# Kernel optimization log

Hardware: AMD Instinct MI355X
Metric: run time of the kernel (lower is better)

Reference implementation:

```python
import jax, jax.numpy as jnp
import numpy as np

T, D = 2048, 1024      # tokens, hidden_size
FF = 512               # moe_intermediate_size
E, K = 16, 4           # num_experts, top_k
L = 3                  # conv_L_cache (short causal conv width)
EPS = 1e-5
SCALE = 1.0            # routed_scaling_factor


def setup_inputs() -> dict:
    key = jax.random.key(0)
    ks = jax.random.split(key, 10)
    s = lambda k, shape, sc: jax.random.normal(k, shape, jnp.float32) * sc
    return {
        "hidden_states": s(ks[0], (T, D), 1.0),
        "residual": s(ks[1], (T, D), 1.0),
        "op_norm_w": jnp.ones((D,), jnp.float32),
        "ffn_norm_w": jnp.ones((D,), jnp.float32),
        "in_proj_w": s(ks[2], (3 * D, D), 0.02),   # produces B, C, x
        "conv_w": s(ks[3], (D, L), 0.2),            # depthwise causal kernel
        "out_proj_w": s(ks[4], (D, D), 0.02),
        "gate_w": s(ks[5], (E, D), 0.02),
        "gate_bias": s(ks[6], (E,), 0.1),           # e_score_correction_bias
        "w1": s(ks[7], (E, 2 * FF, D), 0.02),       # per-expert gate+up
        "w2": s(ks[8], (E, D, FF), 0.02),           # per-expert down
    }


def _fused_add_rmsnorm(x, w, res):
    # vLLM RMSNorm(x, residual): x += residual; residual = x; out = rmsnorm(x)*w
    x = x + res
    res = x
    v = jnp.mean(x * x, axis=-1, keepdims=True)
    return x * jax.lax.rsqrt(v + EPS) * w, res


def reference(hidden_states, residual, op_norm_w, ffn_norm_w, in_proj_w,
              conv_w, out_proj_w, gate_w, gate_bias, w1, w2):
    h, residual = _fused_add_rmsnorm(hidden_states, op_norm_w, residual)

    # ---- ShortConv mixer: Bx = B*x, causal depthwise conv, gate by C ----
    bcx = h @ in_proj_w.T                         # [T, 3D]
    B, C, x = jnp.split(bcx, 3, axis=-1)
    Bx = B * x
    xp = jnp.pad(Bx, ((L - 1, 0), (0, 0)))        # causal left-pad
    shifts = jnp.stack([xp[k:k + T] for k in range(L)], axis=0)  # [L,T,D]
    conv = jnp.einsum('ltd,dl->td', shifts, conv_w)
    y = (C * conv) @ out_proj_w.T                 # [T, D]

    h, residual = _fused_add_rmsnorm(y, ffn_norm_w, residual)

    # ---- Sparse MoE: sigmoid scoring + bias-corrected top-k, renormalize ----
    logits = h.astype(jnp.float32) @ gate_w.T     # [T, E]
    scores = jax.nn.sigmoid(logits)
    choice = scores + gate_bias                   # selection uses biased scores
    _, topi = jax.lax.top_k(choice, K)            # [T, K]
    w = jnp.take_along_axis(scores, topi, axis=-1)  # weights from raw scores
    w = w / (jnp.sum(w, axis=-1, keepdims=True) + 1e-20)  # norm_topk_prob
    cw = jnp.sum(jax.nn.one_hot(topi, E, dtype=h.dtype) * w[..., None].astype(h.dtype), axis=1)  # [T, E]

    # dense dispatch (reference): all experts on all tokens, masked combine
    gu = jnp.einsum('td,efd->etf', h, w1)         # [E, T, 2FF]
    g, u = jnp.split(gu, 2, axis=-1)
    act = jax.nn.silu(g) * u                      # SiluAndMul
    ye = jnp.einsum('etf,edf->etd', act, w2)      # [E, T, D]
    out = jnp.einsum('te,etd->td', cw, ye) * SCALE
    return out, residual
```

## Files before the change

kernel.cpp:

```cpp
#include <hip/hip_runtime.h>
#include <hip/hip_bf16.h>

#define T_  2048
#define D_  1024
#define FF_ 512
#define E_  16
#define K_  4
#define L_  3
static constexpr float EPS = 1e-5f;

typedef __hip_bfloat16 bf16;
typedef __attribute__((ext_vector_type(8))) short bf16x8;
typedef __attribute__((ext_vector_type(4))) float f32x4;

__device__ __forceinline__ float b2f(bf16 x) { return __bfloat162float(x); }

__device__ __forceinline__ unsigned int pk2(float a, float b) {
    __hip_bfloat162 h = __float22bfloat162_rn(make_float2(a, b));
    unsigned int u; __builtin_memcpy(&u, &h, 4); return u;
}

__device__ __forceinline__ void gload_lds16(const bf16* g, bf16* l) {
    __builtin_amdgcn_global_load_lds(
        (const __attribute__((address_space(1))) unsigned int*)g,
        (__attribute__((address_space(3))) unsigned int*)l, 16, 0, 0);
}

__device__ __forceinline__ void split_pack(float4 v, uint2 &hi, uint2 &lo) {
    __hip_bfloat162 h01 = __float22bfloat162_rn(make_float2(v.x, v.y));
    __hip_bfloat162 h23 = __float22bfloat162_rn(make_float2(v.z, v.w));
    float2 r01 = make_float2(v.x - __bfloat162float(h01.x), v.y - __bfloat162float(h01.y));
    float2 r23 = make_float2(v.z - __bfloat162float(h23.x), v.w - __bfloat162float(h23.y));
    __hip_bfloat162 l01 = __float22bfloat162_rn(r01);
    __hip_bfloat162 l23 = __float22bfloat162_rn(r23);
    __builtin_memcpy(&hi.x, &h01, 4); __builtin_memcpy(&hi.y, &h23, 4);
    __builtin_memcpy(&lo.x, &l01, 4); __builtin_memcpy(&lo.y, &l23, 4);
}

__global__ __launch_bounds__(256) void k_convert(const float* __restrict__ w1,
                                                 const float* __restrict__ w2,
                                                 const float* __restrict__ ipw,
                                                 const float* __restrict__ opw,
                                                 bf16* __restrict__ w1b,
                                                 bf16* __restrict__ w2b,
                                                 bf16* __restrict__ iph,
                                                 bf16* __restrict__ ipl,
                                                 bf16* __restrict__ oph,
                                                 bf16* __restrict__ opl) {
    const size_t n1 = (size_t)E_ * 2 * FF_ * D_;
    const size_t n2 = (size_t)E_ * D_ * FF_;
    const size_t n3 = (size_t)3 * D_ * D_;
    const size_t n4 = (size_t)D_ * D_;
    size_t i = ((size_t)blockIdx.x * 256 + threadIdx.x) * 4;
    if (i < n1) {
        float4 v = *(const float4*)&w1[i];
        uint2 h; h.x = pk2(v.x, v.y); h.y = pk2(v.z, v.w);
        *(uint2*)&w1b[i] = h;
    } else if (i < n1 + n2) {
        size_t j = i - n1;
        float4 v = *(const float4*)&w2[j];
        uint2 h; h.x = pk2(v.x, v.y); h.y = pk2(v.z, v.w);
        *(uint2*)&w2b[j] = h;
    } else if (i < n1 + n2 + n3) {
        size_t j = i - n1 - n2;
        float4 v = *(const float4*)&ipw[j];
        uint2 hi, lo; split_pack(v, hi, lo);
        *(uint2*)&iph[j] = hi;
        *(uint2*)&ipl[j] = lo;
    } else if (i < n1 + n2 + n3 + n4) {
        size_t j = i - n1 - n2 - n3;
        float4 v = *(const float4*)&opw[j];
        uint2 hi, lo; split_pack(v, hi, lo);
        *(uint2*)&oph[j] = hi;
        *(uint2*)&opl[j] = lo;
    }
}

__global__ __launch_bounds__(256) void k_zero4(float4* __restrict__ p, int n4) {
    int i = blockIdx.x * 256 + threadIdx.x;
    if (i < n4) p[i] = make_float4(0.f, 0.f, 0.f, 0.f);
}

__device__ __forceinline__ float blockReduceSum(float v) {
    #pragma unroll
    for (int off = 32; off > 0; off >>= 1) v += __shfl_down(v, off, 64);
    __shared__ float s[4];
    __shared__ float tot;
    int lane = threadIdx.x & 63, wid = threadIdx.x >> 6;
    if (lane == 0) s[wid] = v;
    __syncthreads();
    if (threadIdx.x == 0) tot = s[0] + s[1] + s[2] + s[3];
    __syncthreads();
    return tot;
}

__global__ __launch_bounds__(256) void k_addnorm1(const float* __restrict__ x,
                                                  const float* __restrict__ r,
                                                  const float* __restrict__ w,
                                                  bf16* __restrict__ hhi,
                                                  bf16* __restrict__ hlo,
                                                  float* __restrict__ res) {
    int t = blockIdx.x, tid = threadIdx.x;
    float v[4]; float ss = 0.f;
    #pragma unroll
    for (int i = 0; i < 4; i++) {
        int d = tid + 256 * i;
        float s = x[(size_t)t * D_ + d] + r[(size_t)t * D_ + d];
        v[i] = s; ss += s * s;
    }
    float tot = blockReduceSum(ss);
    float rs = rsqrtf(tot / (float)D_ + EPS);
    #pragma unroll
    for (int i = 0; i < 4; i++) {
        int d = tid + 256 * i;
        res[(size_t)t * D_ + d] = v[i];
        float val = v[i] * rs * w[d];
        bf16 hi = __float2bfloat16(val);
        hhi[(size_t)t * D_ + d] = hi;
        hlo[(size_t)t * D_ + d] = __float2bfloat16(val - b2f(hi));
    }
}

__global__ __launch_bounds__(256) void k_addnorm2(const float* __restrict__ y,
                                                  float* __restrict__ res,
                                                  const float* __restrict__ w,
                                                  float* __restrict__ h2,
                                                  bf16* __restrict__ h2b) {
    int t = blockIdx.x, tid = threadIdx.x;
    float v[4]; float ss = 0.f;
    #pragma unroll
    for (int i = 0; i < 4; i++) {
        int d = tid + 256 * i;
        float s = y[(size_t)t * D_ + d] + res[(size_t)t * D_ + d];
        v[i] = s; ss += s * s;
    }
    float tot = blockReduceSum(ss);
    float rs = rsqrtf(tot / (float)D_ + EPS);
    #pragma unroll
    for (int i = 0; i < 4; i++) {
        int d = tid + 256 * i;
        res[(size_t)t * D_ + d] = v[i];
        float val = v[i] * rs * w[d];
        h2[(size_t)t * D_ + d]  = val;
        h2b[(size_t)t * D_ + d] = __float2bfloat16(val);
    }
}

template<int TN>
__global__ __launch_bounds__(256) void k_gemm_small(const bf16* __restrict__ Ah,
                                                    const bf16* __restrict__ Al,
                                                    const bf16* __restrict__ Bh,
                                                    const bf16* __restrict__ Bl,
                                                    float* __restrict__ C,
                                                    int M, int N, int K) {
    constexpr int NF = TN / 64;
    __shared__ bf16 Ash[64 * 32];
    __shared__ bf16 Asl[64 * 32];
    __shared__ bf16 Bsh[TN * 32];
    __shared__ bf16 Bsl[TN * 32];
    int m0 = blockIdx.y * 64, n0 = blockIdx.x * TN;
    int tid = threadIdx.x;
    int wave = tid >> 6, lane = tid & 63, ml = lane & 15, quad = lane >> 4;
    int wn = wave * (TN / 4);
    int r0 = tid >> 2, q0 = tid & 3;
    int c0 = (q0 ^ ((r0 >> 1) & 3)) << 3;
    const bf16* sAh0 = Ah + (size_t)(m0 + r0) * K + c0;
    const bf16* sAl0 = Al + (size_t)(m0 + r0) * K + c0;
    const bf16* sBh0 = Bh + (size_t)(n0 + r0) * K + c0;
    const bf16* sBl0 = Bl + (size_t)(n0 + r0) * K + c0;
    int r1 = r0 + 64;
    int c1 = (q0 ^ ((r1 >> 1) & 3)) << 3;
    const bf16* sBh1 = Bh + (size_t)(n0 + r1) * K + c1;
    const bf16* sBl1 = Bl + (size_t)(n0 + r1) * K + c1;
    int dst0 = wave * 512, dst1 = 2048 + wave * 512;
    int offA[4], offB[NF];
    #pragma unroll
    for (int i = 0; i < 4; i++) {
        int ra = i * 16 + ml;
        offA[i] = ra * 32 + ((quad ^ ((ra >> 1) & 3)) << 3);
    }
    #pragma unroll
    for (int j = 0; j < NF; j++) {
        int rb = wn + j * 16 + ml;
        offB[j] = rb * 32 + ((quad ^ ((rb >> 1) & 3)) << 3);
    }
    f32x4 acc[4][NF] = {};
    for (int kt = 0; kt < K; kt += 32) {
        gload_lds16(sAh0 + kt, Ash + dst0);
        gload_lds16(sAl0 + kt, Asl + dst0);
        gload_lds16(sBh0 + kt, Bsh + dst0);
        gload_lds16(sBl0 + kt, Bsl + dst0);
        if constexpr (TN == 128) {
            gload_lds16(sBh1 + kt, Bsh + dst1);
            gload_lds16(sBl1 + kt, Bsl + dst1);
        }
        __syncthreads();
        bf16x8 ah[4], al[4], bh[NF], bl[NF];
        #pragma unroll
        for (int i = 0; i < 4; i++) {
            ah[i] = *(const bf16x8*)&Ash[offA[i]];
            al[i] = *(const bf16x8*)&Asl[offA[i]];
        }
        #pragma unroll
        for (int j = 0; j < NF; j++) {
            bh[j] = *(const bf16x8*)&Bsh[offB[j]];
            bl[j] = *(const bf16x8*)&Bsl[offB[j]];
        }
        #pragma unroll
        for (int i = 0; i < 4; i++)
            #pragma unroll
            for (int j = 0; j < NF; j++) {
                acc[i][j] = __builtin_amdgcn_mfma_f32_16x16x32_bf16(ah[i], bh[j], acc[i][j], 0, 0, 0);
                acc[i][j] = __builtin_amdgcn_mfma_f32_16x16x32_bf16(al[i], bh[j], acc[i][j], 0, 0, 0);
                acc[i][j] = __builtin_amdgcn_mfma_f32_16x16x32_bf16(ah[i], bl[j], acc[i][j], 0, 0, 0);
            }
        __syncthreads();
    }
    #pragma unroll
    for (int i = 0; i < 4; i++)
        #pragma unroll
        for (int j = 0; j < NF; j++)
            #pragma unroll
            for (int r = 0; r < 4; r++) {
                int row = m0 + i * 16 + quad * 4 + r;
                int col = n0 + wn + j * 16 + ml;
                C[(size_t)row * N + col] = acc[i][j][r];
            }
}

__global__ __launch_bounds__(256) void k_gemm_split(const bf16* __restrict__ Ah,
                                                    const bf16* __restrict__ Al,
                                                    const float* __restrict__ B,
                                                    float* __restrict__ C,
                                                    int M, int N, int K) {
    __shared__ bf16 Ash[128][40];
    __shared__ bf16 Asl[128][40];
    __shared__ bf16 Bsh[128][40];
    __shared__ bf16 Bsl[128][40];
    int m0 = blockIdx.y * 128, n0 = blockIdx.x * 128;
    int tid = threadIdx.x;
    int wave = tid >> 6, lane = tid & 63, ml = lane & 15, quad = lane >> 4;
    int wm = (wave >> 1) * 64, wn = (wave & 1) * 64;
    f32x4 acc[4][4] = {};
    for (int kt = 0; kt < K; kt += 32) {
        #pragma unroll
        for (int p = 0; p < 2; p++) {
            int ch = p * 256 + tid, row = ch >> 2, c8 = (ch & 3) << 3;
            *(uint4*)&Ash[row][c8] = *(const uint4*)&Ah[(size_t)(m0 + row) * K + kt + c8];
            *(uint4*)&Asl[row][c8] = *(const uint4*)&Al[(size_t)(m0 + row) * K + kt + c8];
        }
        #pragma unroll
        for (int p = 0; p < 4; p++) {
            int ch = p * 256 + tid, row = ch >> 3, c4 = (ch & 7) << 2;
            float4 v = *(const float4*)&B[(size_t)(n0 + row) * K + kt + c4];
            uint2 hi, lo; split_pack(v, hi, lo);
            *(uint2*)&Bsh[row][c4] = hi;
            *(uint2*)&Bsl[row][c4] = lo;
        }
        __syncthreads();
        bf16x8 ah[4], al[4], bh[4], bl[4];
        #pragma unroll
        for (int i = 0; i < 4; i++) {
            ah[i] = *(const bf16x8*)&Ash[wm + i * 16 + ml][quad * 8];
            al[i] = *(const bf16x8*)&Asl[wm + i * 16 + ml][quad * 8];
        }
        #pragma unroll
        for (int j = 0; j < 4; j++) {
            bh[j] = *(const bf16x8*)&Bsh[wn + j * 16 + ml][quad * 8];
            bl[j] = *(const bf16x8*)&Bsl[wn + j * 16 + ml][quad * 8];
        }
        #pragma unroll
        for (int i = 0; i < 4; i++)
            #pragma unroll
            for (int j = 0; j < 4; j++) {
                acc[i][j] = __builtin_amdgcn_mfma_f32_16x16x32_bf16(ah[i], bh[j], acc[i][j], 0, 0, 0);
                acc[i][j] = __builtin_amdgcn_mfma_f32_16x16x32_bf16(al[i], bh[j], acc[i][j], 0, 0, 0);
                acc[i][j] = __builtin_amdgcn_mfma_f32_16x16x32_bf16(ah[i], bl[j], acc[i][j], 0, 0, 0);
            }
        __syncthreads();
    }
    #pragma unroll
    for (int i = 0; i < 4; i++)
        #pragma unroll
        for (int j = 0; j < 4; j++)
            #pragma unroll
            for (int r = 0; r < 4; r++) {
                int row = m0 + wm + i * 16 + quad * 4 + r;
                int col = n0 + wn + j * 16 + ml;
                C[(size_t)row * N + col] = acc[i][j][r];
            }
}

__global__ __launch_bounds__(256) void k_conv(const float* __restrict__ bcx,
                                              const float* __restrict__ cw,
                                              bf16* __restrict__ cchi,
                                              bf16* __restrict__ cclo) {
    int t = blockIdx.x, tid = threadIdx.x;
    #pragma unroll
    for (int i = 0; i < 4; i++) {
        int d = tid + 256 * i;
        float acc = 0.f;
        #pragma unroll
        for (int l = 0; l < L_; l++) {
            int tt = t + l - (L_ - 1);
            if (tt >= 0) {
                float bb = bcx[(size_t)tt * 3 * D_ + d];
                float xx = bcx[(size_t)tt * 3 * D_ + 2 * D_ + d];
                acc += bb * xx * cw[d * L_ + l];
            }
        }
        float c = bcx[(size_t)t * 3 * D_ + D_ + d];
        float val = c * acc;
        bf16 hi = __float2bfloat16(val);
        cchi[(size_t)t * D_ + d] = hi;
        cclo[(size_t)t * D_ + d] = __float2bfloat16(val - b2f(hi));
    }
}

__global__ __launch_bounds__(256) void k_gate(const float* __restrict__ h2,
                                              const float* __restrict__ gw,
                                              const float* __restrict__ gb,
                                              int4* __restrict__ choice_idx,
                                              float4* __restrict__ choice_wgt) {
    int t = blockIdx.x, tid = threadIdx.x;
    __shared__ float hs[D_];
    __shared__ float logits[E_];
    #pragma unroll
    for (int i = 0; i < 4; i++) { int d = tid + 256 * i; hs[d] = h2[(size_t)t * D_ + d]; }
    __syncthreads();
    int e = tid >> 4, j = tid & 15;
    float p = 0.f;
    for (int d = j; d < D_; d += 16) p += hs[d] * gw[(size_t)e * D_ + d];
    #pragma unroll
    for (int off = 8; off > 0; off >>= 1) p += __shfl_down(p, off, 64);
    if (j == 0) logits[e] = p;
    __syncthreads();
    if (tid == 0) {
        float sc[E_], ch[E_];
        #pragma unroll
        for (int i = 0; i < E_; i++) {
            float s = 1.f / (1.f + expf(-logits[i]));
            sc[i] = s; ch[i] = s + gb[i];
        }
        int idx[K_]; float wv[K_]; float wsum = 0.f;
        bool used[E_] = {};
        #pragma unroll
        for (int k = 0; k < K_; k++) {
            int best = 0; float bv = -1e30f;
            for (int i = 0; i < E_; i++)
                if (!used[i] && ch[i] > bv) { bv = ch[i]; best = i; }
            used[best] = true; idx[k] = best; wv[k] = sc[best]; wsum += sc[best];
        }
        float inv = 1.f / (wsum + 1e-20f);
        choice_idx[t] = make_int4(idx[0], idx[1], idx[2], idx[3]);
        choice_wgt[t] = make_float4(wv[0] * inv, wv[1] * inv, wv[2] * inv, wv[3] * inv);
    }
}

__global__ __launch_bounds__(256) void k_scatter(const int4* __restrict__ choice_idx,
                                                 const float4* __restrict__ choice_wgt,
                                                 int* __restrict__ cnt,
                                                 int* __restrict__ tok_list,
                                                 float* __restrict__ tok_w) {
    int e = blockIdx.x;
    __shared__ int ctr;
    if (threadIdx.x == 0) ctr = 0;
    __syncthreads();
    int lane = threadIdx.x & 63;
    for (int t = threadIdx.x; t < T_; t += 256) {
        int4   ci = choice_idx[t];
        float4 cw = choice_wgt[t];
        bool m = false; float w = 0.f;
        if (ci.x == e) { m = true; w = cw.x; }
        else if (ci.y == e) { m = true; w = cw.y; }
        else if (ci.z == e) { m = true; w = cw.z; }
        else if (ci.w == e) { m = true; w = cw.w; }
        unsigned long long mask = __ballot(m);
        int loff = __popcll(mask & ((1ull << lane) - 1ull));
        int wcnt = __popcll(mask);
        int base = 0;
        if (lane == 0 && wcnt > 0) base = atomicAdd(&ctr, wcnt);
        base = __shfl(base, 0, 64);
        if (m) {
            tok_list[e * T_ + base + loff] = t;
            tok_w[e * T_ + base + loff]    = w;
        }
    }
    __syncthreads();
    if (threadIdx.x == 0) cnt[e] = ctr;
}

__global__ void k_scan(const int* __restrict__ cnt, int* __restrict__ off) {
    if (threadIdx.x == 0) {
        int s = 0;
        for (int e = 0; e < E_; e++) { off[e] = s; s += min(cnt[e], T_); }
        off[E_] = s;
    }
}

__global__ __launch_bounds__(256) void k_moe_w1_pre(const bf16* __restrict__ h2,
                                                    const bf16* __restrict__ w1b,
                                                    const int* __restrict__ cnt,
                                                    const int* __restrict__ off,
                                                    const int* __restrict__ tok_list,
                                                    bf16* __restrict__ act) {
    int e = blockIdx.y >> 4, mt = blockIdx.y & 15;
    int m0 = mt * 128;
    int nt = min(cnt[e], T_);
    if (m0 >= nt) return;
    int n0 = blockIdx.x * 64;
    int base = off[e];
    __shared__ bf16 As[128 * 32];
    __shared__ bf16 Bg[64 * 32];
    __shared__ bf16 Bu[64 * 32];
    int tid = threadIdx.x;
    int wave = tid >> 6, lane = tid & 63, ml = lane & 15, quad = lane >> 4;
    int wm = wave * 32;
    const bf16* w1e = w1b + (size_t)e * 2 * FF_ * D_;
    int r0 = tid >> 2, q0 = tid & 3, r1 = r0 + 64;
    int c0 = (q0 ^ ((r0 >> 1) & 3)) << 3;
    int c1 = (q0 ^ ((r1 >> 1) & 3)) << 3;
    int ma0 = m0 + r0, ma1 = m0 + r1;
    int tok0 = tok_list[e * T_ + (ma0 < nt ? ma0 : 0)] & (T_ - 1);
    int tok1 = tok_list[e * T_ + (ma1 < nt ? ma1 : 0)] & (T_ - 1);
    const bf16* sA0 = h2 + (size_t)tok0 * D_ + c0;
    const bf16* sA1 = h2 + (size_t)tok1 * D_ + c1;
    const bf16* sBg = w1e + (size_t)(n0 + r0) * D_ + c0;
    const bf16* sBu = w1e + (size_t)(FF_ + n0 + r0) * D_ + c0;
    int dst0 = wave * 512, dst1 = 2048 + wave * 512;
    int offA[2], offB[4];
    #pragma unroll
    for (int i = 0; i < 2; i++) {
        int r = wm + i * 16 + ml;
        offA[i] = r * 32 + ((quad ^ ((r >> 1) & 3)) << 3);
    }
    #pragma unroll
    for (int j = 0; j < 4; j++) {
        int r = j * 16 + ml;
        offB[j] = r * 32 + ((quad ^ ((r >> 1) & 3)) << 3);
    }
    f32x4 ag[2][4] = {}, au[2][4] = {};
    for (int kt = 0; kt < D_; kt += 32) {
        gload_lds16(sA0 + kt, As + dst0);
        gload_lds16(sA1 + kt, As + dst1);
        gload_lds16(sBg + kt, Bg + dst0);
        gload_lds16(sBu + kt, Bu + dst0);
        __syncthreads();
        bf16x8 a[2], bg[4], bu[4];
        #pragma unroll
        for (int i = 0; i < 2; i++) a[i] = *(const bf16x8*)&As[offA[i]];
        #pragma unroll
        for (int j = 0; j < 4; j++) {
            bg[j] = *(const bf16x8*)&Bg[offB[j]];
            bu[j] = *(const bf16x8*)&Bu[offB[j]];
        }
        #pragma unroll
        for (int i = 0; i < 2; i++)
            #pragma unroll
            for (int j = 0; j < 4; j++) {
                ag[i][j] = __builtin_amdgcn_mfma_f32_16x16x32_bf16(a[i], bg[j], ag[i][j], 0, 0, 0);
                au[i][j] = __builtin_amdgcn_mfma_f32_16x16x32_bf16(a[i], bu[j], au[i][j], 0, 0, 0);
            }
        __syncthreads();
    }
    #pragma unroll
    for (int i = 0; i < 2; i++)
        #pragma unroll
        for (int j = 0; j < 4; j++)
            #pragma unroll
            for (int r = 0; r < 4; r++) {
                int m = m0 + wm + i * 16 + quad * 4 + r;
                if (m < nt) {
                    float g = ag[i][j][r], u = au[i][j][r];
                    float a = g / (1.f + __expf(-g)) * u;
                    act[(size_t)(base + m) * FF_ + n0 + j * 16 + ml] = __float2bfloat16(a);
                }
            }
}

__global__ __launch_bounds__(256) void k_moe_w1(const bf16* __restrict__ h2,
                                                const float* __restrict__ w1,
                                                const int* __restrict__ cnt,
                                                const int* __restrict__ off,
                                                const int* __restrict__ tok_list,
                                                bf16* __restrict__ act) {
    int e = blockIdx.y >> 4, mt = blockIdx.y & 15;
    int m0 = mt * 128;
    int nt = min(cnt[e], T_);
    if (m0 >= nt) return;
    int n0 = blockIdx.x * 64;
    int base = off[e];
    __shared__ bf16 As[128][40];
    __shared__ bf16 Bg[64][40];
    __shared__ bf16 Bu[64][40];
    __shared__ int  toks[128];
    int tid = threadIdx.x;
    if (tid < 128) {
        int m = m0 + tid;
        toks[tid] = ((m < nt) ? tok_list[e * T_ + m] : tok_list[e * T_]) & (T_ - 1);
    }
    __syncthreads();
    const float* w1e = w1 + (size_t)e * 2 * FF_ * D_;
    int wave = tid >> 6, lane = tid & 63, ml = lane & 15, quad = lane >> 4;
    int wm = wave * 32;
    f32x4 ag[2][4] = {}, au[2][4] = {};
    for (int kt = 0; kt < D_; kt += 32) {
        #pragma unroll
        for (int p = 0; p < 2; p++) {
            int ch = p * 256 + tid, row = ch >> 2, c8 = (ch & 3) << 3;
            *(uint4*)&As[row][c8] = *(const uint4*)&h2[(size_t)toks[row] * D_ + kt + c8];
        }
        #pragma unroll
        for (int p = 0; p < 2; p++) {
            int ch = p * 256 + tid, row = ch >> 3, c4 = (ch & 7) << 2;
            float4 vg = *(const float4*)&w1e[(size_t)(n0 + row) * D_ + kt + c4];
            float4 vu = *(const float4*)&w1e[(size_t)(FF_ + n0 + row) * D_ + kt + c4];
            uint2 wg; wg.x = pk2(vg.x, vg.y); wg.y = pk2(vg.z, vg.w);
            uint2 wu; wu.x = pk2(vu.x, vu.y); wu.y = pk2(vu.z, vu.w);
            *(uint2*)&Bg[row][c4] = wg;
            *(uint2*)&Bu[row][c4] = wu;
        }
        __syncthreads();
        bf16x8 a[2], bg[4], bu[4];
        #pragma unroll
        for (int i = 0; i < 2; i++) a[i] = *(const bf16x8*)&As[wm + i * 16 + ml][quad * 8];
        #pragma unroll
        for (int j = 0; j < 4; j++) {
            bg[j] = *(const bf16x8*)&Bg[j * 16 + ml][quad * 8];
            bu[j] = *(const bf16x8*)&Bu[j * 16 + ml][quad * 8];
        }
        #pragma unroll
        for (int i = 0; i < 2; i++)
            #pragma unroll
            for (int j = 0; j < 4; j++) {
                ag[i][j] = __builtin_amdgcn_mfma_f32_16x16x32_bf16(a[i], bg[j], ag[i][j], 0, 0, 0);
                au[i][j] = __builtin_amdgcn_mfma_f32_16x16x32_bf16(a[i], bu[j], au[i][j], 0, 0, 0);
            }
        __syncthreads();
    }
    #pragma unroll
    for (int i = 0; i < 2; i++)
        #pragma unroll
        for (int j = 0; j < 4; j++)
            #pragma unroll
            for (int r = 0; r < 4; r++) {
                int m = m0 + wm + i * 16 + quad * 4 + r;
                if (m < nt) {
                    float g = ag[i][j][r], u = au[i][j][r];
                    float a = g / (1.f + __expf(-g)) * u;
                    act[(size_t)(base + m) * FF_ + n0 + j * 16 + ml] = __float2bfloat16(a);
                }
            }
}

__global__ __launch_bounds__(256) void k_moe_w2_pre(const bf16* __restrict__ act,
                                                    const bf16* __restrict__ w2b,
                                                    const int* __restrict__ cnt,
                                                    const int* __restrict__ off,
                                                    const int* __restrict__ tok_list,
                                                    const float* __restrict__ tok_w,
                                                    float* __restrict__ out0) {
    int e = blockIdx.y >> 4, mt = blockIdx.y & 15;
    int m0 = mt * 128;
    int nt = min(cnt[e], T_);
    if (m0 >= nt) return;
    int n0 = blockIdx.x * 128;
    int base = off[e];
    __shared__ bf16 As[128 * 32];
    __shared__ bf16 Bs[128 * 32];
    int tid = threadIdx.x;
    int wave = tid >> 6, lane = tid & 63, ml = lane & 15, quad = lane >> 4;
    int wm = (wave >> 1) * 64, wn = (wave & 1) * 64;
    const bf16* w2e = w2b + (size_t)e * D_ * FF_;
    int r0 = tid >> 2, q0 = tid & 3, r1 = r0 + 64;
    int c0 = (q0 ^ ((r0 >> 1) & 3)) << 3;
    int c1 = (q0 ^ ((r1 >> 1) & 3)) << 3;
    const bf16* sA0 = act + (size_t)(base + m0 + r0) * FF_ + c0;
    const bf16* sA1 = act + (size_t)(base + m0 + r1) * FF_ + c1;
    const bf16* sB0 = w2e + (size_t)(n0 + r0) * FF_ + c0;
    const bf16* sB1 = w2e + (size_t)(n0 + r1) * FF_ + c1;
    int dst0 = wave * 512, dst1 = 2048 + wave * 512;
    int offA[4], offB[4];
    #pragma unroll
    for (int i = 0; i < 4; i++) {
        int ra = wm + i * 16 + ml;
        offA[i] = ra * 32 + ((quad ^ ((ra >> 1) & 3)) << 3);
        int rb = wn + i * 16 + ml;
        offB[i] = rb * 32 + ((quad ^ ((rb >> 1) & 3)) << 3);
    }
    f32x4 acc[4][4] = {};
    for (int kt = 0; kt < FF_; kt += 32) {
        gload_lds16(sA0 + kt, As + dst0);
        gload_lds16(sA1 + kt, As + dst1);
        gload_lds16(sB0 + kt, Bs + dst0);
        gload_lds16(sB1 + kt, Bs + dst1);
        __syncthreads();
        bf16x8 a[4], b[4];
        #pragma unroll
        for (int i = 0; i < 4; i++) {
            a[i] = *(const bf16x8*)&As[offA[i]];
            b[i] = *(const bf16x8*)&Bs[offB[i]];
        }
        #pragma unroll
        for (int i = 0; i < 4; i++)
            #pragma unroll
            for (int j = 0; j < 4; j++)
                acc[i][j] = __builtin_amdgcn_mfma_f32_16x16x32_bf16(a[i], b[j], acc[i][j], 0, 0, 0);
        __syncthreads();
    }
    #pragma unroll
    for (int i = 0; i < 4; i++)
        #pragma unroll
        for (int r = 0; r < 4; r++) {
            int m = m0 + wm + i * 16 + quad * 4 + r;
            if (m < nt) {
                int   tok = tok_list[e * T_ + m] & (T_ - 1);
                float wgt = tok_w[e * T_ + m];
                #pragma unroll
                for (int j = 0; j < 4; j++) {
                    int col = n0 + wn + j * 16 + ml;
                    atomicAdd(&out0[(size_t)tok * D_ + col], wgt * acc[i][j][r]);
                }
            }
        }
}

__global__ __launch_bounds__(256) void k_moe_w2(const bf16* __restrict__ act,
                                                const float* __restrict__ w2,
                                                const int* __restrict__ cnt,
                                                const int* __restrict__ off,
                                                const int* __restrict__ tok_list,
                                                const float* __restrict__ tok_w,
                                                float* __restrict__ out0) {
    int e = blockIdx.y >> 4, mt = blockIdx.y & 15;
    int m0 = mt * 128;
    int nt = min(cnt[e], T_);
    if (m0 >= nt) return;
    int n0 = blockIdx.x * 128;
    int base = off[e];
    __shared__ bf16 As[128][40];
    __shared__ bf16 Bs[128][40];
    int tid = threadIdx.x;
    int wave = tid >> 6, lane = tid & 63, ml = lane & 15, quad = lane >> 4;
    int wm = (wave >> 1) * 64, wn = (wave & 1) * 64;
    const float* w2e = w2 + (size_t)e * D_ * FF_;
    f32x4 acc[4][4] = {};
    for (int kt = 0; kt < FF_; kt += 32) {
        #pragma unroll
        for (int p = 0; p < 2; p++) {
            int ch = p * 256 + tid, row = ch >> 2, c8 = (ch & 3) << 3;
            uint4 v = make_uint4(0, 0, 0, 0);
            if (m0 + row < nt) v = *(const uint4*)&act[(size_t)(base + m0 + row) * FF_ + kt + c8];
            *(uint4*)&As[row][c8] = v;
        }
        #pragma unroll
        for (int p = 0; p < 4; p++) {
            int ch = p * 256 + tid, row = ch >> 3, c4 = (ch & 7) << 2;
            float4 v = *(const float4*)&w2e[(size_t)(n0 + row) * FF_ + kt + c4];
            uint2 w; w.x = pk2(v.x, v.y); w.y = pk2(v.z, v.w);
            *(uint2*)&Bs[row][c4] = w;
        }
        __syncthreads();
        bf16x8 a[4], b[4];
        #pragma unroll
        for (int i = 0; i < 4; i++) a[i] = *(const bf16x8*)&As[wm + i * 16 + ml][quad * 8];
        #pragma unroll
        for (int j = 0; j < 4; j++) b[j] = *(const bf16x8*)&Bs[wn + j * 16 + ml][quad * 8];
        #pragma unroll
        for (int i = 0; i < 4; i++)
            #pragma unroll
            for (int j = 0; j < 4; j++)
                acc[i][j] = __builtin_amdgcn_mfma_f32_16x16x32_bf16(a[i], b[j], acc[i][j], 0, 0, 0);
        __syncthreads();
    }
    #pragma unroll
    for (int i = 0; i < 4; i++)
        #pragma unroll
        for (int r = 0; r < 4; r++) {
            int m = m0 + wm + i * 16 + quad * 4 + r;
            if (m < nt) {
                int   tok = tok_list[e * T_ + m] & (T_ - 1);
                float wgt = tok_w[e * T_ + m];
                #pragma unroll
                for (int j = 0; j < 4; j++) {
                    int col = n0 + wn + j * 16 + ml;
                    atomicAdd(&out0[(size_t)tok * D_ + col], wgt * acc[i][j][r]);
                }
            }
        }
}

extern "C" void kernel_launch(void* const* d_in, const int* in_sizes, int n_in,
                              void* d_out, int out_size, void* d_ws, size_t ws_size,
                              hipStream_t stream) {
    const float* hidden     = (const float*)d_in[0];
    const float* residual   = (const float*)d_in[1];
    const float* op_norm_w  = (const float*)d_in[2];
    const float* ffn_norm_w = (const float*)d_in[3];
    const float* in_proj_w  = (const float*)d_in[4];
    const float* conv_w     = (const float*)d_in[5];
    const float* out_proj_w = (const float*)d_in[6];
    const float* gate_w     = (const float*)d_in[7];
    const float* gate_bias  = (const float*)d_in[8];
    const float* w1         = (const float*)d_in[9];
    const float* w2         = (const float*)d_in[10];

    char* p = (char*)d_ws;
    int*    cnt        = (int*)p;        p += 256;
    int*    off        = (int*)p;        p += 128;
    int*    tok_list   = (int*)p;        p += (size_t)E_ * T_ * 4;
    float*  tok_w      = (float*)p;      p += (size_t)E_ * T_ * 4;
    int4*   choice_idx = (int4*)p;       p += (size_t)T_ * 16;
    float4* choice_wgt = (float4*)p;     p += (size_t)T_ * 16;
    char*   regA       = p;              p += (size_t)T_ * D_ * 2 * 2;
    char*   regB       = p;              p += (size_t)T_ * 3 * D_ * 4;

    const size_t n1 = (size_t)E_ * 2 * FF_ * D_;
    const size_t n2 = (size_t)E_ * D_ * FF_;
    const size_t n3 = (size_t)3 * D_ * D_;
    const size_t n4 = (size_t)D_ * D_;
    bf16* w1b = (bf16*)p;  p += n1 * 2;
    bf16* w2b = (bf16*)p;  p += n2 * 2;
    bf16* iph = (bf16*)p;  p += n3 * 2;
    bf16* ipl = (bf16*)p;  p += n3 * 2;
    bf16* oph = (bf16*)p;  p += n4 * 2;
    bf16* opl = (bf16*)p;  p += n4 * 2;
    bool pre = ((size_t)(p - (char*)d_ws) <= ws_size);

    bf16* h1hi = (bf16*)regA;
    bf16* h1lo = (bf16*)(regA + (size_t)T_ * D_ * 2);
    bf16* cchi = h1hi;
    bf16* cclo = h1lo;
    bf16* act  = (bf16*)regA;
    float* bcx = (float*)regB;
    float* y   = (float*)regB;
    float* h2  = (float*)(regB + (size_t)T_ * D_ * 4);
    bf16*  h2b = (bf16*)(regB + (size_t)T_ * D_ * 8);

    float* out0 = (float*)d_out;
    float* res  = out0 + (size_t)T_ * D_;

    if (pre) {
        int nq = (int)((n1 + n2 + n3 + n4) / 4 / 256);
        k_convert<<<nq, 256, 0, stream>>>(w1, w2, in_proj_w, out_proj_w,
                                          w1b, w2b, iph, ipl, oph, opl);
    }
    k_zero4<<<(T_ * D_ / 4 + 255) / 256, 256, 0, stream>>>((float4*)out0, T_ * D_ / 4);
    k_addnorm1<<<T_, 256, 0, stream>>>(hidden, residual, op_norm_w, h1hi, h1lo, res);
    if (pre)
        k_gemm_small<128><<<dim3(3 * D_ / 128, T_ / 64), 256, 0, stream>>>(
            h1hi, h1lo, iph, ipl, bcx, T_, 3 * D_, D_);
    else
        k_gemm_split<<<dim3(3 * D_ / 128, T_ / 128), 256, 0, stream>>>(
            h1hi, h1lo, in_proj_w, bcx, T_, 3 * D_, D_);
    k_conv<<<T_, 256, 0, stream>>>(bcx, conv_w, cchi, cclo);
    if (pre)
        k_gemm_small<64><<<dim3(D_ / 64, T_ / 64), 256, 0, stream>>>(
            cchi, cclo, oph, opl, y, T_, D_, D_);
    else
        k_gemm_split<<<dim3(D_ / 128, T_ / 128), 256, 0, stream>>>(
            cchi, cclo, out_proj_w, y, T_, D_, D_);
    k_addnorm2<<<T_, 256, 0, stream>>>(y, res, ffn_norm_w, h2, h2b);
    k_gate<<<T_, 256, 0, stream>>>(h2, gate_w, gate_bias, choice_idx, choice_wgt);
    k_scatter<<<E_, 256, 0, stream>>>(choice_idx, choice_wgt, cnt, tok_list, tok_w);
    k_scan<<<1, 64, 0, stream>>>(cnt, off);
    if (pre) {
        k_moe_w1_pre<<<dim3(FF_ / 64, E_ * (T_ / 128)), 256, 0, stream>>>(
            h2b, w1b, cnt, off, tok_list, act);
        k_moe_w2_pre<<<dim3(D_ / 128, E_ * (T_ / 128)), 256, 0, stream>>>(
            act, w2b, cnt, off, tok_list, tok_w, out0);
    } else {
        k_moe_w1<<<dim3(FF_ / 64, E_ * (T_ / 128)), 256, 0, stream>>>(
            h2b, w1, cnt, off, tok_list, act);
        k_moe_w2<<<dim3(D_ / 128, E_ * (T_ / 128)), 256, 0, stream>>>(
            act, w2, cnt, off, tok_list, tok_w, out0);
    }
}
```

Measured before the change: 393.4 us.

## Double-buffer LDS tiles and remap workgroups in split-bf16 projection GEMMs

Replaces the single-buffered projection GEMM with a double-buffered version that issues global-to-LDS loads for the next K tile while MFMAs run on the current one, halving the number of barrier-separated load/compute phases. It also remaps block IDs in a round-robin stride of 8, presumably to spread neighbouring tiles across XCDs for better L2 locality, and makes K a compile-time constant. The cost is twice the LDS per block, which may lower occupancy.

```diff
diff --git a/kernel.cpp b/kernel.cpp
--- a/kernel.cpp
+++ b/kernel.cpp
@@ -146,32 +146,35 @@
     }
 }
 
-template<int TN>
-__global__ __launch_bounds__(256) void k_gemm_small(const bf16* __restrict__ Ah,
-                                                    const bf16* __restrict__ Al,
-                                                    const bf16* __restrict__ Bh,
-                                                    const bf16* __restrict__ Bl,
-                                                    float* __restrict__ C,
-                                                    int M, int N, int K) {
+template<int TN, int KK>
+__global__ __launch_bounds__(256) void k_gemm_db(const bf16* __restrict__ Ah,
+                                                 const bf16* __restrict__ Al,
+                                                 const bf16* __restrict__ Bh,
+                                                 const bf16* __restrict__ Bl,
+                                                 float* __restrict__ C,
+                                                 int M, int N) {
     constexpr int NF = TN / 64;
-    __shared__ bf16 Ash[64 * 32];
-    __shared__ bf16 Asl[64 * 32];
-    __shared__ bf16 Bsh[TN * 32];
-    __shared__ bf16 Bsl[TN * 32];
-    int m0 = blockIdx.y * 64, n0 = blockIdx.x * TN;
+    __shared__ bf16 Ash0[64 * 32], Asl0[64 * 32], Bsh0[TN * 32], Bsl0[TN * 32];
+    __shared__ bf16 Ash1[64 * 32], Asl1[64 * 32], Bsh1[TN * 32], Bsl1[TN * 32];
+    int nwg = gridDim.x * gridDim.y;
+    int bid = blockIdx.y * gridDim.x + blockIdx.x;
+    int cpx = nwg >> 3;
+    int logical = (bid & 7) * cpx + (bid >> 3);
+    int ly = logical % gridDim.y, lx = logical / gridDim.y;
+    int m0 = ly * 64, n0 = lx * TN;
     int tid = threadIdx.x;
     int wave = tid >> 6, lane = tid & 63, ml = lane & 15, quad = lane >> 4;
     int wn = wave * (TN / 4);
     int r0 = tid >> 2, q0 = tid & 3;
     int c0 = (q0 ^ ((r0 >> 1) & 3)) << 3;
-    const bf16* sAh0 = Ah + (size_t)(m0 + r0) * K + c0;
-    const bf16* sAl0 = Al + (size_t)(m0 + r0) * K + c0;
-    const bf16* sBh0 = Bh + (size_t)(n0 + r0) * K + c0;
-    const bf16* sBl0 = Bl + (size_t)(n0 + r0) * K + c0;
+    const bf16* sAh0 = Ah + (size_t)(m0 + r0) * KK + c0;
+    const bf16* sAl0 = Al + (size_t)(m0 + r0) * KK + c0;
+    const bf16* sBh0 = Bh + (size_t)(n0 + r0) * KK + c0;
+    const bf16* sBl0 = Bl + (size_t)(n0 + r0) * KK + c0;
     int r1 = r0 + 64;
     int c1 = (q0 ^ ((r1 >> 1) & 3)) << 3;
-    const bf16* sBh1 = Bh + (size_t)(n0 + r1) * K + c1;
-    const bf16* sBl1 = Bl + (size_t)(n0 + r1) * K + c1;
+    const bf16* sBh1 = Bh + (size_t)(n0 + r1) * KK + c1;
+    const bf16* sBl1 = Bl + (size_t)(n0 + r1) * KK + c1;
     int dst0 = wave * 512, dst1 = 2048 + wave * 512;
     int offA[4], offB[NF];
     #pragma unroll
@@ -185,26 +188,27 @@
         offB[j] = rb * 32 + ((quad ^ ((rb >> 1) & 3)) << 3);
     }
     f32x4 acc[4][NF] = {};
-    for (int kt = 0; kt < K; kt += 32) {
-        gload_lds16(sAh0 + kt, Ash + dst0);
-        gload_lds16(sAl0 + kt, Asl + dst0);
-        gload_lds16(sBh0 + kt, Bsh + dst0);
-        gload_lds16(sBl0 + kt, Bsl + dst0);
+    auto stage = [&](bf16* aH, bf16* aL, bf16* bH, bf16* bL, int kt) {
+        gload_lds16(sAh0 + kt, aH + dst0);
+        gload_lds16(sAl0 + kt, aL + dst0);
+        gload_lds16(sBh0 + kt, bH + dst0);
+        gload_lds16(sBl0 + kt, bL + dst0);
         if constexpr (TN == 128) {
-            gload_lds16(sBh1 + kt, Bsh + dst1);
-            gload_lds16(sBl1 + kt, Bsl + dst1);
-        }
-        __syncthreads();
+            gload_lds16(sBh1 + kt, bH + dst1);
+            gload_lds16(sBl1 + kt, bL + dst1);
+        }
+    };
+    auto compute = [&](const bf16* aH, const bf16* aL, const bf16* bH, const bf16* bL) {
         bf16x8 ah[4], al[4], bh[NF], bl[NF];
         #pragma unroll
         for (int i = 0; i < 4; i++) {
-            ah[i] = *(const bf16x8*)&Ash[offA[i]];
-            al[i] = *(const bf16x8*)&Asl[offA[i]];
+            ah[i] = *(const bf16x8*)&aH[offA[i]];
+            al[i] = *(const bf16x8*)&aL[offA[i]];
         }
         #pragma unroll
         for (int j = 0; j < NF; j++) {
-            bh[j] = *(const bf16x8*)&Bsh[offB[j]];
-            bl[j] = *(const bf16x8*)&Bsl[offB[j]];
+            bh[j] = *(const bf16x8*)&bH[offB[j]];
+            bl[j] = *(const bf16x8*)&bL[offB[j]];
         }
         #pragma unroll
         for (int i = 0; i < 4; i++)
@@ -214,6 +218,18 @@
                 acc[i][j] = __builtin_amdgcn_mfma_f32_16x16x32_bf16(al[i], bh[j], acc[i][j], 0, 0, 0);
                 acc[i][j] = __builtin_amdgcn_mfma_f32_16x16x32_bf16(ah[i], bl[j], acc[i][j], 0, 0, 0);
             }
+    };
+    constexpr int PAIRS = (KK / 32) / 2;
+    static_assert((KK / 32) % 2 == 0, "even tile count required");
+    stage(Ash0, Asl0, Bsh0, Bsl0, 0);
+    __syncthreads();
+    for (int p = 0; p < PAIRS; p++) {
+        bool lastp = (p == PAIRS - 1);
+        stage(Ash1, Asl1, Bsh1, Bsl1, (2 * p + 1) * 32);
+        compute(Ash0, Asl0, Bsh0, Bsl0);
+        __syncthreads();
+        if (!lastp) stage(Ash0, Asl0, Bsh0, Bsl0, (2 * p + 2) * 32);
+        compute(Ash1, Asl1, Bsh1, Bsl1);
         __syncthreads();
     }
     #pragma unroll
@@ -748,15 +764,15 @@
     k_zero4<<<(T_ * D_ / 4 + 255) / 256, 256, 0, stream>>>((float4*)out0, T_ * D_ / 4);
     k_addnorm1<<<T_, 256, 0, stream>>>(hidden, residual, op_norm_w, h1hi, h1lo, res);
     if (pre)
-        k_gemm_small<128><<<dim3(3 * D_ / 128, T_ / 64), 256, 0, stream>>>(
-            h1hi, h1lo, iph, ipl, bcx, T_, 3 * D_, D_);
+        k_gemm_db<128, 1024><<<dim3(3 * D_ / 128, T_ / 64), 256, 0, stream>>>(
+            h1hi, h1lo, iph, ipl, bcx, T_, 3 * D_);
     else
         k_gemm_split<<<dim3(3 * D_ / 128, T_ / 128), 256, 0, stream>>>(
             h1hi, h1lo, in_proj_w, bcx, T_, 3 * D_, D_);
     k_conv<<<T_, 256, 0, stream>>>(bcx, conv_w, cchi, cclo);
     if (pre)
-        k_gemm_small<64><<<dim3(D_ / 64, T_ / 64), 256, 0, stream>>>(
-            cchi, cclo, oph, opl, y, T_, D_, D_);
+        k_gemm_db<64, 1024><<<dim3(D_ / 64, T_ / 64), 256, 0, stream>>>(
+            cchi, cclo, oph, opl, y, T_, D_);
     else
         k_gemm_split<<<dim3(D_ / 128, T_ / 128), 256, 0, stream>>>(
             cchi, cclo, out_proj_w, y, T_, D_, D_);
```

New measurement: 395.1 us. No clear change (+0.5%).

## Fuse small elementwise kernels and fold the scan into the scatter kernel

Applied to the files above, without the earlier changes.

Folds output zeroing into the first add+RMSNorm kernel and fuses the second add+RMSNorm with the gate/top-k kernel, so the fp32 h2 buffer is no longer written and reread. The expert-offset scan moves into the last-finishing scatter block via an atomic completion counter, and that counter is reset inside the conv kernel. Together these remove three kernel launches and some global traffic. The cost is reliance on atomics and threadfence ordering, and on the counter stored in cnt[31] being reset on every call.

```diff
diff --git a/kernel.cpp b/kernel.cpp
--- a/kernel.cpp
+++ b/kernel.cpp
@@ -76,11 +76,6 @@
     }
 }
 
-__global__ __launch_bounds__(256) void k_zero4(float4* __restrict__ p, int n4) {
-    int i = blockIdx.x * 256 + threadIdx.x;
-    if (i < n4) p[i] = make_float4(0.f, 0.f, 0.f, 0.f);
-}
-
 __device__ __forceinline__ float blockReduceSum(float v) {
     #pragma unroll
     for (int off = 32; off > 0; off >>= 1) v += __shfl_down(v, off, 64);
@@ -94,12 +89,13 @@
     return tot;
 }
 
-__global__ __launch_bounds__(256) void k_addnorm1(const float* __restrict__ x,
-                                                  const float* __restrict__ r,
-                                                  const float* __restrict__ w,
-                                                  bf16* __restrict__ hhi,
-                                                  bf16* __restrict__ hlo,
-                                                  float* __restrict__ res) {
+__global__ __launch_bounds__(256) void k_addnorm1z(const float* __restrict__ x,
+                                                   const float* __restrict__ r,
+                                                   const float* __restrict__ w,
+                                                   bf16* __restrict__ hhi,
+                                                   bf16* __restrict__ hlo,
+                                                   float* __restrict__ res,
+                                                   float* __restrict__ out0) {
     int t = blockIdx.x, tid = threadIdx.x;
     float v[4]; float ss = 0.f;
     #pragma unroll
@@ -107,6 +103,7 @@
         int d = tid + 256 * i;
         float s = x[(size_t)t * D_ + d] + r[(size_t)t * D_ + d];
         v[i] = s; ss += s * s;
+        out0[(size_t)t * D_ + d] = 0.f;
     }
     float tot = blockReduceSum(ss);
     float rs = rsqrtf(tot / (float)D_ + EPS);
@@ -118,31 +115,6 @@
         bf16 hi = __float2bfloat16(val);
         hhi[(size_t)t * D_ + d] = hi;
         hlo[(size_t)t * D_ + d] = __float2bfloat16(val - b2f(hi));
-    }
-}
-
-__global__ __launch_bounds__(256) void k_addnorm2(const float* __restrict__ y,
-                                                  float* __restrict__ res,
-                                                  const float* __restrict__ w,
-                                                  float* __restrict__ h2,
-                                                  bf16* __restrict__ h2b) {
-    int t = blockIdx.x, tid = threadIdx.x;
-    float v[4]; float ss = 0.f;
-    #pragma unroll
-    for (int i = 0; i < 4; i++) {
-        int d = tid + 256 * i;
-        float s = y[(size_t)t * D_ + d] + res[(size_t)t * D_ + d];
-        v[i] = s; ss += s * s;
-    }
-    float tot = blockReduceSum(ss);
-    float rs = rsqrtf(tot / (float)D_ + EPS);
-    #pragma unroll
-    for (int i = 0; i < 4; i++) {
-        int d = tid + 256 * i;
-        res[(size_t)t * D_ + d] = v[i];
-        float val = v[i] * rs * w[d];
-        h2[(size_t)t * D_ + d]  = val;
-        h2b[(size_t)t * D_ + d] = __float2bfloat16(val);
     }
 }
 
@@ -291,11 +263,13 @@
             }
 }
 
-__global__ __launch_bounds__(256) void k_conv(const float* __restrict__ bcx,
-                                              const float* __restrict__ cw,
-                                              bf16* __restrict__ cchi,
-                                              bf16* __restrict__ cclo) {
+__global__ __launch_bounds__(256) void k_conv2(const float* __restrict__ bcx,
+                                               const float* __restrict__ cw,
+                                               bf16* __restrict__ cchi,
+                                               bf16* __restrict__ cclo,
+                                               int* __restrict__ zctl) {
     int t = blockIdx.x, tid = threadIdx.x;
+    if (blockIdx.x == 0 && tid < 32) zctl[tid] = 0;
     #pragma unroll
     for (int i = 0; i < 4; i++) {
         int d = tid + 256 * i;
@@ -317,16 +291,34 @@
     }
 }
 
-__global__ __launch_bounds__(256) void k_gate(const float* __restrict__ h2,
-                                              const float* __restrict__ gw,
-                                              const float* __restrict__ gb,
-                                              int4* __restrict__ choice_idx,
-                                              float4* __restrict__ choice_wgt) {
+__global__ __launch_bounds__(256) void k_an2_gate(const float* __restrict__ y,
+                                                  float* __restrict__ res,
+                                                  const float* __restrict__ w,
+                                                  bf16* __restrict__ h2b,
+                                                  const float* __restrict__ gw,
+                                                  const float* __restrict__ gb,
+                                                  int4* __restrict__ choice_idx,
+                                                  float4* __restrict__ choice_wgt) {
     int t = blockIdx.x, tid = threadIdx.x;
     __shared__ float hs[D_];
     __shared__ float logits[E_];
-    #pragma unroll
-    for (int i = 0; i < 4; i++) { int d = tid + 256 * i; hs[d] = h2[(size_t)t * D_ + d]; }
+    float v[4]; float ss = 0.f;
+    #pragma unroll
+    for (int i = 0; i < 4; i++) {
+        int d = tid + 256 * i;
+        float s = y[(size_t)t * D_ + d] + res[(size_t)t * D_ + d];
+        v[i] = s; ss += s * s;
+    }
+    float tot = blockReduceSum(ss);
+    float rs = rsqrtf(tot / (float)D_ + EPS);
+    #pragma unroll
+    for (int i = 0; i < 4; i++) {
+        int d = tid + 256 * i;
+        res[(size_t)t * D_ + d] = v[i];
+        float val = v[i] * rs * w[d];
+        h2b[(size_t)t * D_ + d] = __float2bfloat16(val);
+        hs[d] = val;
+    }
     __syncthreads();
     int e = tid >> 4, j = tid & 15;
     float p = 0.f;
@@ -357,11 +349,13 @@
     }
 }
 
-__global__ __launch_bounds__(256) void k_scatter(const int4* __restrict__ choice_idx,
-                                                 const float4* __restrict__ choice_wgt,
-                                                 int* __restrict__ cnt,
-                                                 int* __restrict__ tok_list,
-                                                 float* __restrict__ tok_w) {
+__global__ __launch_bounds__(256) void k_scatter2(const int4* __restrict__ choice_idx,
+                                                  const float4* __restrict__ choice_wgt,
+                                                  int* __restrict__ cnt,
+                                                  int* __restrict__ tok_list,
+                                                  float* __restrict__ tok_w,
+                                                  int* __restrict__ off,
+                                                  int* __restrict__ done) {
     int e = blockIdx.x;
     __shared__ int ctr;
     if (threadIdx.x == 0) ctr = 0;
@@ -387,14 +381,18 @@
         }
     }
     __syncthreads();
-    if (threadIdx.x == 0) cnt[e] = ctr;
-}
-
-__global__ void k_scan(const int* __restrict__ cnt, int* __restrict__ off) {
     if (threadIdx.x == 0) {
-        int s = 0;
-        for (int e = 0; e < E_; e++) { off[e] = s; s += min(cnt[e], T_); }
-        off[E_] = s;
+        atomicExch(&cnt[e], ctr);
+        __threadfence();
+        int prev = atomicAdd(done, 1);
+        if (prev == E_ - 1) {
+            int s = 0;
+            for (int i = 0; i < E_; i++) {
+                int c = atomicAdd(&cnt[i], 0);
+                off[i] = s; s += min(c, T_);
+            }
+            off[E_] = s;
+        }
     }
 }
 
@@ -734,7 +732,6 @@
     bf16* act  = (bf16*)regA;
     float* bcx = (float*)regB;
     float* y   = (float*)regB;
-    float* h2  = (float*)(regB + (size_t)T_ * D_ * 4);
     bf16*  h2b = (bf16*)(regB + (size_t)T_ * D_ * 8);
 
     float* out0 = (float*)d_out;
@@ -745,25 +742,24 @@
         k_convert<<<nq, 256, 0, stream>>>(w1, w2, in_proj_w, out_proj_w,
                                           w1b, w2b, iph, ipl, oph, opl);
     }
-    k_zero4<<<(T_ * D_ / 4 + 255) / 256, 256, 0, stream>>>((float4*)out0, T_ * D_ / 4);
-    k_addnorm1<<<T_, 256, 0, stream>>>(hidden, residual, op_norm_w, h1hi, h1lo, res);
+    k_addnorm1z<<<T_, 256, 0, stream>>>(hidden, residual, op_norm_w, h1hi, h1lo, res, out0);
     if (pre)
         k_gemm_small<128><<<dim3(3 * D_ / 128, T_ / 64), 256, 0, stream>>>(
             h1hi, h1lo, iph, ipl, bcx, T_, 3 * D_, D_);
     else
         k_gemm_split<<<dim3(3 * D_ / 128, T_ / 128), 256, 0, stream>>>(
             h1hi, h1lo, in_proj_w, bcx, T_, 3 * D_, D_);
-    k_conv<<<T_, 256, 0, stream>>>(bcx, conv_w, cchi, cclo);
+    k_conv2<<<T_, 256, 0, stream>>>(bcx, conv_w, cchi, cclo, cnt);
     if (pre)
         k_gemm_small<64><<<dim3(D_ / 64, T_ / 64), 256, 0, stream>>>(
             cchi, cclo, oph, opl, y, T_, D_, D_);
     else
         k_gemm_split<<<dim3(D_ / 128, T_ / 128), 256, 0, stream>>>(
             cchi, cclo, out_proj_w, y, T_, D_, D_);
-    k_addnorm2<<<T_, 256, 0, stream>>>(y, res, ffn_norm_w, h2, h2b);
-    k_gate<<<T_, 256, 0, stream>>>(h2, gate_w, gate_bias, choice_idx, choice_wgt);
-    k_scatter<<<E_, 256, 0, stream>>>(choice_idx, choice_wgt, cnt, tok_list, tok_w);
-    k_scan<<<1, 64, 0, stream>>>(cnt, off);
+    k_an2_gate<<<T_, 256, 0, stream>>>(y, res, ffn_norm_w, h2b, gate_w, gate_bias,
+                                       choice_idx, choice_wgt);
+    k_scatter2<<<E_, 256, 0, stream>>>(choice_idx, choice_wgt, cnt, tok_list, tok_w,
+                                       off, &cnt[31]);
     if (pre) {
         k_moe_w1_pre<<<dim3(FF_ / 64, E_ * (T_ / 128)), 256, 0, stream>>>(
             h2b, w1b, cnt, off, tok_list, act);
```

Result: no change. 395.9 us (+0.6%).
